# Kernel optimization log

Measured on AMD Instinct MI355X. Metric: run time of the kernel, lower is better.

The kernel has to match this reference:

```python
import jax, jax.numpy as jnp
import numpy as np

VISION_TOKEN_TYPE = 1
HIDDEN = 4096
INTER = 11008


def setup_inputs() -> dict:
    key = jax.random.key(0)
    ks = jax.random.split(key, 8)
    B, L, D, F = 2, 2048, HIDDEN, INTER
    s_in = 1.0 / np.sqrt(D)
    s_mid = 1.0 / np.sqrt(F)
    inp = {
        "hidden_states": jax.random.normal(ks[0], (B, L, D), dtype=jnp.float32),
        "token_type_ids": jax.random.randint(ks[1], (B, L), 0, 2, dtype=jnp.int64),
        # language expert weights (stored as [in, out] for x @ W)
        "lang_gate": jax.random.normal(ks[2], (D, F), dtype=jnp.float32) * s_in,
        "lang_up": jax.random.normal(ks[3], (D, F), dtype=jnp.float32) * s_in,
        "lang_down": jax.random.normal(ks[4], (F, D), dtype=jnp.float32) * s_mid,
        # vision expert weights
        "vis_gate": jax.random.normal(ks[5], (D, F), dtype=jnp.float32) * s_in,
        "vis_up": jax.random.normal(ks[6], (D, F), dtype=jnp.float32) * s_in,
        "vis_down": jax.random.normal(ks[7], (F, D), dtype=jnp.float32) * s_mid,
    }
    return inp


def _swiglu_mlp(x, w_gate, w_up, w_down):
    # x: (B, L, D) -> (B, L, D)
    return (jax.nn.silu(x @ w_gate) * (x @ w_up)) @ w_down


def _vision_mask(token_type_ids):
    # vision token i is one whose type AND next token's type are VISION_TOKEN_TYPE;
    # last position is always language.
    is_vis = token_type_ids == VISION_TOKEN_TYPE
    pair = is_vis[:, :-1] & is_vis[:, 1:]
    return jnp.pad(pair, ((0, 0), (0, 1)), constant_values=False)  # (B, L) bool


def reference(hidden_states, token_type_ids, lang_gate, lang_up, lang_down,
              vis_gate, vis_up, vis_down):
    vision_mask = _vision_mask(token_type_ids)  # (B, L)
    out_vis = _swiglu_mlp(hidden_states, vis_gate, vis_up, vis_down)
    out_lang = _swiglu_mlp(hidden_states, lang_gate, lang_up, lang_down)
    return jnp.where(vision_mask[..., None], out_vis, out_lang)
```

## Files before the change

kernel.cpp:

```cpp
#include <hip/hip_runtime.h>
#include <cstdint>

#define HD 4096
#define FF 11008
#define BB 2
#define LL 2048
#define BL (BB*LL)
#define NN 86
#define MB1 17
#define MB2 17

using bf16x8  = __attribute__((ext_vector_type(8))) __bf16;
using f32x4   = __attribute__((ext_vector_type(4))) float;
using ushort8 = __attribute__((ext_vector_type(8))) unsigned short;

__device__ __forceinline__ int imin(int a, int b) { return a < b ? a : b; }

__device__ __forceinline__ unsigned short f2bf(float f) {
  union { float f; unsigned u; } v; v.f = f;
  unsigned r = v.u + 0x7fffu + ((v.u >> 16) & 1u);
  return (unsigned short)(r >> 16);
}

__device__ __forceinline__ void gld_lds16(const void* g, void* l) {
  __builtin_amdgcn_global_load_lds(
      (__attribute__((address_space(1))) void*)g,
      (__attribute__((address_space(3))) void*)l, 16, 0, 0);
}

__global__ void detect_mode(const int* __restrict__ w, int* __restrict__ flag) {
  int acc = 0;
  for (int i = 1 + 2 * (int)threadIdx.x; i < BL; i += 512) acc |= w[i];
  if (acc != 0) atomicOr(flag, 1);
}

__global__ void mask_compact(const int* __restrict__ w, const int* __restrict__ flag,
                             int* __restrict__ cnts, int* __restrict__ idxL,
                             int* __restrict__ idxV) {
  int i = blockIdx.x * 256 + threadIdx.x;
  if (i >= BL) return;
  int p = i & (LL - 1);
  bool i32 = (*flag != 0);
  int ti = i32 ? w[i] : w[2 * i];
  bool vis = false;
  if (p < LL - 1) {
    int tn = i32 ? w[i + 1] : w[2 * (i + 1)];
    vis = (ti == 1) && (tn == 1);
  }
  if (vis) idxV[atomicAdd(&cnts[1], 1)] = i;
  else     idxL[atomicAdd(&cnts[0], 1)] = i;
}

__global__ void convx(const float* __restrict__ x, unsigned short* __restrict__ xb) {
  size_t i = ((size_t)blockIdx.x * 256 + threadIdx.x) * 8;
  float4 a = *(const float4*)(x + i);
  float4 b = *(const float4*)(x + i + 4);
  ushort8 o;
  o[0] = f2bf(a.x); o[1] = f2bf(a.y); o[2] = f2bf(a.z); o[3] = f2bf(a.w);
  o[4] = f2bf(b.x); o[5] = f2bf(b.y); o[6] = f2bf(b.z); o[7] = f2bf(b.w);
  *(ushort8*)(xb + i) = o;
}

__global__ __launch_bounds__(256) void convTW(const float* __restrict__ in,
                                              unsigned short* __restrict__ out,
                                              int K, int N, int toff) {
  __shared__ unsigned short T[64 * 260];
  const int n0 = blockIdx.x * 256, k0 = blockIdx.y * 64;
  const int t = threadIdx.x, w = t >> 6, l = t & 63;
#pragma unroll
  for (int it = 0; it < 16; ++it) {
    int k = it * 4 + w;
    float4 v = *(const float4*)(in + (size_t)(k0 + k) * N + n0 + l * 4);
    unsigned lo = (unsigned)f2bf(v.x) | ((unsigned)f2bf(v.y) << 16);
    unsigned hi = (unsigned)f2bf(v.z) | ((unsigned)f2bf(v.w) << 16);
    *(uint2*)&T[k * 260 + l * 4] = make_uint2(lo, hi);
  }
  __syncthreads();
  const int gn = n0 + t;
  size_t r = (toff < 0) ? (size_t)gn
                        : (size_t)(((gn >> 4) << 5) + toff + (gn & 15));
  unsigned short* op = out + r * K + k0;
#pragma unroll
  for (int c = 0; c < 8; ++c) {
    ushort8 o;
#pragma unroll
    for (int j = 0; j < 8; ++j) o[j] = T[(c * 8 + j) * 260 + t];
    *(ushort8*)(op + c * 8) = o;
  }
}

#define BAR()  __builtin_amdgcn_s_barrier()
#define VMC(n) asm volatile("s_waitcnt vmcnt(" #n ")" ::: "memory")
#define LGK0() asm volatile("s_waitcnt lgkmcnt(0)" ::: "memory")

#define STG_A(h, kt) { \
  gld_lds16(aptr[h][0] + (size_t)(kt) * 64, &lds[(((kt) & 1) << 14) + ((h) << 13) + w * 512]); \
  gld_lds16(aptr[h][1] + (size_t)(kt) * 64, &lds[(((kt) & 1) << 14) + ((h) << 13) + (w + 8) * 512]); }
#define STG_B(h, kt) { \
  gld_lds16(bptr[h][0] + (size_t)(kt) * 64, &lds[32768 + (((kt) & 1) << 14) + ((h) << 13) + w * 512]); \
  gld_lds16(bptr[h][1] + (size_t)(kt) * 64, &lds[32768 + (((kt) & 1) << 14) + ((h) << 13) + (w + 8) * 512]); }

#define RD_A(s, rh) { _Pragma("unroll") \
  for (int mi = 0; mi < 4; ++mi) { \
    a[mi][0] = *(const bf16x8*)&lds[((s) << 14) + addrA[rh][mi]]; \
    a[mi][1] = *(const bf16x8*)&lds[((s) << 14) + (addrA[rh][mi] ^ 32)]; } }
#define RD_B(s, ch, br) { _Pragma("unroll") \
  for (int ni = 0; ni < 2; ++ni) { \
    br[ni][0] = *(const bf16x8*)&lds[((s) << 14) + addrB[ch][ni]]; \
    br[ni][1] = *(const bf16x8*)&lds[((s) << 14) + (addrB[ch][ni] ^ 32)]; } }

#define MFMA_Q(rh, br, ch) { \
  __builtin_amdgcn_s_setprio(1); \
  _Pragma("unroll") for (int mi = 0; mi < 4; ++mi) \
  _Pragma("unroll") for (int ni = 0; ni < 2; ++ni) { \
    acc[(rh)*4+mi][(ch)*2+ni] = __builtin_amdgcn_mfma_f32_16x16x32_bf16(a[mi][0], br[ni][0], acc[(rh)*4+mi][(ch)*2+ni], 0, 0, 0); \
    acc[(rh)*4+mi][(ch)*2+ni] = __builtin_amdgcn_mfma_f32_16x16x32_bf16(a[mi][1], br[ni][1], acc[(rh)*4+mi][(ch)*2+ni], 0, 0, 0); } \
  __builtin_amdgcn_s_setprio(0); }

#define KLOOP_8PH(KEXT) \
  STG_A(0, 0); STG_A(1, 0); STG_B(0, 0); STG_B(1, 0); \
  STG_B(0, 1); STG_B(1, 1); \
  VMC(4); BAR(); \
  for (int i = 0; i < (KEXT) / 128 - 1; ++i) { \
    const int kt1 = 2 * i + 1, kt2 = 2 * i + 2, kt3 = 2 * i + 3; \
    RD_A(0, 0); RD_B(0, 0, b0); STG_A(0, kt1); BAR(); LGK0(); \
    MFMA_Q(0, b0, 0); BAR(); \
    RD_B(0, 1, b1); STG_A(1, kt1); BAR(); LGK0(); \
    MFMA_Q(0, b1, 1); BAR(); \
    RD_A(0, 1); STG_B(0, kt2); BAR(); LGK0(); \
    MFMA_Q(1, b0, 0); BAR(); \
    STG_B(1, kt2); VMC(4); BAR(); \
    MFMA_Q(1, b1, 1); BAR(); \
    RD_A(1, 0); RD_B(1, 0, b0); STG_A(0, kt2); BAR(); LGK0(); \
    MFMA_Q(0, b0, 0); BAR(); \
    RD_B(1, 1, b1); STG_A(1, kt2); BAR(); LGK0(); \
    MFMA_Q(0, b1, 1); BAR(); \
    RD_A(1, 1); STG_B(0, kt3); BAR(); LGK0(); \
    MFMA_Q(1, b0, 0); BAR(); \
    STG_B(1, kt3); VMC(4); BAR(); \
    MFMA_Q(1, b1, 1); BAR(); \
  } \
  { \
    const int kt1 = (KEXT) / 64 - 1; \
    RD_A(0, 0); RD_B(0, 0, b0); STG_A(0, kt1); BAR(); LGK0(); \
    MFMA_Q(0, b0, 0); BAR(); \
    RD_B(0, 1, b1); STG_A(1, kt1); BAR(); LGK0(); \
    MFMA_Q(0, b1, 1); BAR(); \
    RD_A(0, 1); BAR(); LGK0(); \
    MFMA_Q(1, b0, 0); BAR(); \
    VMC(0); BAR(); \
    MFMA_Q(1, b1, 1); BAR(); \
    RD_A(1, 0); RD_B(1, 0, b0); BAR(); LGK0(); \
    MFMA_Q(0, b0, 0); BAR(); \
    RD_B(1, 1, b1); BAR(); LGK0(); \
    MFMA_Q(0, b1, 1); BAR(); \
    RD_A(1, 1); BAR(); LGK0(); \
    MFMA_Q(1, b0, 0); BAR(); \
    BAR(); \
    MFMA_Q(1, b1, 1); BAR(); \
  }

__global__ __launch_bounds__(512, 2) void gemm1m_8ph(
    const unsigned short* __restrict__ Xb,
    const unsigned short* __restrict__ Wgu0, const unsigned short* __restrict__ Wgu1,
    const int* __restrict__ idxL, const int* __restrict__ idxV,
    const int* __restrict__ cnts, unsigned short* __restrict__ H) {
  const int orig = blockIdx.x;
  const int xcd = orig & 7;
  const int pos = orig >> 3;
  const int wgid = xcd * 183 + pos;
  const int bx = wgid / MB1;
  int mb = wgid - bx * MB1;
  if (bx >= NN) return;
  const int cntL = cnts[0], cntV = cnts[1];
  const int nL = (cntL + 255) >> 8;
  const int* idx; const unsigned short* Wgu; int cnt;
  if (mb < nL) { idx = idxL; Wgu = Wgu0; cnt = cntL; }
  else {
    mb -= nL;
    if (mb >= ((cntV + 255) >> 8)) return;
    idx = idxV; Wgu = Wgu1; cnt = cntV;
  }
  const int m0 = mb << 8;

  __shared__ __align__(16) unsigned short lds[65536];

  const int t = threadIdx.x, l = t & 63, w = t >> 6;
  const int wr = w >> 2, wc = w & 3;
  const int srcswz = (((l & 7) ^ (l >> 3)) << 3);

  const unsigned short* aptr[2][2];
  const unsigned short* bptr[2][2];
#pragma unroll
  for (int h = 0; h < 2; ++h)
#pragma unroll
    for (int j = 0; j < 2; ++j) {
      int r = h * 128 + (w + j * 8) * 8 + (l >> 3);
      int tok = idx[imin(m0 + r, cnt - 1)];
      aptr[h][j] = Xb + (size_t)tok * HD + srcswz;
      bptr[h][j] = Wgu + (size_t)(bx * 256 + r) * HD + srcswz;
    }

  const int koff0 = (((l >> 4) ^ (l & 7)) << 3);
  int addrA[2][4], addrB[2][2];
#pragma unroll
  for (int rh = 0; rh < 2; ++rh)
#pragma unroll
    for (int mi = 0; mi < 4; ++mi)
      addrA[rh][mi] = (wr * 128 + rh * 64 + mi * 16 + (l & 15)) * 64 + koff0;
#pragma unroll
  for (int ch = 0; ch < 2; ++ch)
#pragma unroll
    for (int ni = 0; ni < 2; ++ni)
      addrB[ch][ni] = 32768 + (wc * 64 + ch * 32 + ni * 16 + (l & 15)) * 64 + koff0;

  f32x4 acc[8][4] = {};
  bf16x8 a[4][2], b0[2][2], b1[2][2];

  KLOOP_8PH(HD)

#pragma unroll
  for (int mi = 0; mi < 8; ++mi)
#pragma unroll
    for (int j = 0; j < 4; ++j) {
      int grow = m0 + wr * 128 + mi * 16 + ((l >> 4) << 2) + j;
      if (grow < cnt) {
        int token = idx[grow];
#pragma unroll
        for (int pair = 0; pair < 2; ++pair) {
          float g = acc[mi][pair * 2][j];
          float u = acc[mi][pair * 2 + 1][j];
          float h = (g / (1.f + __expf(-g))) * u;
          int f = bx * 128 + wc * 32 + pair * 16 + (l & 15);
          H[(size_t)token * FF + f] = f2bf(h);
        }
      }
    }
}

__global__ __launch_bounds__(512, 2) void gemm2_8ph(
    const unsigned short* __restrict__ Hh,
    const unsigned short* __restrict__ Wd0, const unsigned short* __restrict__ Wd1,
    const int* __restrict__ idxL, const int* __restrict__ idxV,
    const int* __restrict__ cnts, float* __restrict__ Out) {
  const int orig = blockIdx.x;
  const int xcd = orig & 7;
  const int pos = orig >> 3;
  const int wgid = xcd * ((HD / 256) * MB2 / 8) + pos;
  const int bx = wgid / MB2;
  int mb = wgid - bx * MB2;
  const int cntL = cnts[0], cntV = cnts[1];
  const int nL = (cntL + 255) >> 8;
  const int* idx; const unsigned short* Wd; int cnt;
  if (mb < nL) { idx = idxL; Wd = Wd0; cnt = cntL; }
  else {
    mb -= nL;
    if (mb >= ((cntV + 255) >> 8)) return;
    idx = idxV; Wd = Wd1; cnt = cntV;
  }
  const int m0 = mb << 8;

  __shared__ __align__(16) unsigned short lds[65536];

  const int t = threadIdx.x, l = t & 63, w = t >> 6;
  const int wr = w >> 2, wc = w & 3;
  const int srcswz = (((l & 7) ^ (l >> 3)) << 3);

  const unsigned short* aptr[2][2];
  const unsigned short* bptr[2][2];
#pragma unroll
  for (int h = 0; h < 2; ++h)
#pragma unroll
    for (int j = 0; j < 2; ++j) {
      int r = h * 128 + (w + j * 8) * 8 + (l >> 3);
      int tok = idx[imin(m0 + r, cnt - 1)];
      aptr[h][j] = Hh + (size_t)tok * FF + srcswz;
      bptr[h][j] = Wd + (size_t)(bx * 256 + r) * FF + srcswz;
    }

  const int koff0 = (((l >> 4) ^ (l & 7)) << 3);
  int addrA[2][4], addrB[2][2];
#pragma unroll
  for (int rh = 0; rh < 2; ++rh)
#pragma unroll
    for (int mi = 0; mi < 4; ++mi)
      addrA[rh][mi] = (wr * 128 + rh * 64 + mi * 16 + (l & 15)) * 64 + koff0;
#pragma unroll
  for (int ch = 0; ch < 2; ++ch)
#pragma unroll
    for (int ni = 0; ni < 2; ++ni)
      addrB[ch][ni] = 32768 + (wc * 64 + ch * 32 + ni * 16 + (l & 15)) * 64 + koff0;

  f32x4 acc[8][4] = {};
  bf16x8 a[4][2], b0[2][2], b1[2][2];

  KLOOP_8PH(FF)

#pragma unroll
  for (int mi = 0; mi < 8; ++mi)
#pragma unroll
    for (int j = 0; j < 4; ++j) {
      int grow = m0 + wr * 128 + mi * 16 + ((l >> 4) << 2) + j;
      if (grow < cnt) {
        int token = idx[grow];
        size_t base = (size_t)token * HD + bx * 256 + wc * 64 + (l & 15);
#pragma unroll
        for (int nf = 0; nf < 4; ++nf)
          Out[base + nf * 16] = acc[mi][nf][j];
      }
    }
}

extern "C" void kernel_launch(void* const* d_in, const int* in_sizes, int n_in,
                              void* d_out, int out_size, void* d_ws, size_t ws_size,
                              hipStream_t stream) {
  const float* hs = (const float*)d_in[0];
  const int*   tt = (const int*)d_in[1];
  const float* lg = (const float*)d_in[2];
  const float* lu = (const float*)d_in[3];
  const float* ld = (const float*)d_in[4];
  const float* vg = (const float*)d_in[5];
  const float* vu = (const float*)d_in[6];
  const float* vd = (const float*)d_in[7];
  float* out = (float*)d_out;
  char* ws = (char*)d_ws;

  int* cnts = (int*)ws;
  int* flag = (int*)(ws + 8);
  int* idxL = (int*)(ws + 1024);
  int* idxV = (int*)(ws + 1024 + BL * 4);
  unsigned short* Xb   = (unsigned short*)(ws + 65536);
  unsigned short* Hb   = Xb + (size_t)BL * HD;
  unsigned short* Wgu0 = Hb + (size_t)BL * FF;
  unsigned short* Wgu1 = Wgu0 + (size_t)2 * HD * FF;
  unsigned short* Wd0  = Wgu0;
  unsigned short* Wd1  = Wgu0 + (size_t)HD * FF;

  hipMemsetAsync(ws, 0, 64, stream);
  detect_mode<<<1, 256, 0, stream>>>(tt, flag);
  mask_compact<<<BL / 256, 256, 0, stream>>>(tt, flag, cnts, idxL, idxV);
  convx<<<(BL * HD / 8) / 256, 256, 0, stream>>>(hs, Xb);

  convTW<<<dim3(FF / 256, HD / 64), 256, 0, stream>>>(lg, Wgu0, HD, FF, 0);
  convTW<<<dim3(FF / 256, HD / 64), 256, 0, stream>>>(lu, Wgu0, HD, FF, 16);
  convTW<<<dim3(FF / 256, HD / 64), 256, 0, stream>>>(vg, Wgu1, HD, FF, 0);
  convTW<<<dim3(FF / 256, HD / 64), 256, 0, stream>>>(vu, Wgu1, HD, FF, 16);
  gemm1m_8ph<<<dim3(8 * 183), 512, 0, stream>>>(Xb, Wgu0, Wgu1, idxL, idxV, cnts, Hb);

  convTW<<<dim3(HD / 256, FF / 64), 256, 0, stream>>>(ld, Wd0, FF, HD, -1);
  convTW<<<dim3(HD / 256, FF / 64), 256, 0, stream>>>(vd, Wd1, FF, HD, -1);
  gemm2_8ph<<<dim3((HD / 256) * MB2), 512, 0, stream>>>(Hb, Wd0, Wd1, idxL, idxV, cnts, out);
}
```

Before: 1.580 ms.

## Split-K the down-projection GEMM in two and add a reduction pass

```diff
diff --git a/kernel.cpp b/kernel.cpp
--- a/kernel.cpp
+++ b/kernel.cpp
@@ -9,6 +9,7 @@
 #define NN 86
 #define MB1 17
 #define MB2 17
+#define KS2 5504
 
 using bf16x8  = __attribute__((ext_vector_type(8))) __bf16;
 using f32x4   = __attribute__((ext_vector_type(4))) float;
@@ -61,32 +62,41 @@
   *(ushort8*)(xb + i) = o;
 }
 
-__global__ __launch_bounds__(256) void convTW(const float* __restrict__ in,
-                                              unsigned short* __restrict__ out,
-                                              int K, int N, int toff) {
-  __shared__ unsigned short T[64 * 260];
-  const int n0 = blockIdx.x * 256, k0 = blockIdx.y * 64;
-  const int t = threadIdx.x, w = t >> 6, l = t & 63;
-#pragma unroll
-  for (int it = 0; it < 16; ++it) {
-    int k = it * 4 + w;
-    float4 v = *(const float4*)(in + (size_t)(k0 + k) * N + n0 + l * 4);
-    unsigned lo = (unsigned)f2bf(v.x) | ((unsigned)f2bf(v.y) << 16);
-    unsigned hi = (unsigned)f2bf(v.z) | ((unsigned)f2bf(v.w) << 16);
-    *(uint2*)&T[k * 260 + l * 4] = make_uint2(lo, hi);
+__global__ void convT(const float* __restrict__ in, unsigned short* __restrict__ out,
+                      int K, int N, int toff) {
+  __shared__ unsigned short T[64][65];
+  int n0 = blockIdx.x * 64, k0 = blockIdx.y * 64;
+  int t = threadIdx.x;
+  int cg = (t & 15) * 4;
+  int r0 = t >> 4;
+#pragma unroll
+  for (int it = 0; it < 4; ++it) {
+    int r = r0 + it * 16;
+    float4 v = *(const float4*)(in + (size_t)(k0 + r) * N + n0 + cg);
+    T[cg + 0][r] = f2bf(v.x); T[cg + 1][r] = f2bf(v.y);
+    T[cg + 2][r] = f2bf(v.z); T[cg + 3][r] = f2bf(v.w);
   }
   __syncthreads();
-  const int gn = n0 + t;
-  size_t r = (toff < 0) ? (size_t)gn
-                        : (size_t)(((gn >> 4) << 5) + toff + (gn & 15));
-  unsigned short* op = out + r * K + k0;
-#pragma unroll
-  for (int c = 0; c < 8; ++c) {
+  int nl = t >> 3, kg = t & 7;
+#pragma unroll
+  for (int it = 0; it < 2; ++it) {
+    int n = nl + it * 32;
     ushort8 o;
 #pragma unroll
-    for (int j = 0; j < 8; ++j) o[j] = T[(c * 8 + j) * 260 + t];
-    *(ushort8*)(op + c * 8) = o;
-  }
+    for (int j = 0; j < 8; ++j) o[j] = T[n][kg * 8 + j];
+    int gn = n0 + n;
+    size_t r = (toff < 0) ? (size_t)gn
+                          : (size_t)(((gn >> 4) << 5) + toff + (gn & 15));
+    *(ushort8*)(out + r * K + k0 + kg * 8) = o;
+  }
+}
+
+__global__ void reduce2(const float* __restrict__ P, float* __restrict__ out) {
+  size_t i = ((size_t)blockIdx.x * 256 + threadIdx.x) * 4;
+  float4 a = *(const float4*)(P + i);
+  float4 b = *(const float4*)(P + (size_t)BL * HD + i);
+  float4 o = make_float4(a.x + b.x, a.y + b.y, a.z + b.z, a.w + b.w);
+  *(float4*)(out + i) = o;
 }
 
 #define BAR()  __builtin_amdgcn_s_barrier()
@@ -242,13 +252,15 @@
     const unsigned short* __restrict__ Hh,
     const unsigned short* __restrict__ Wd0, const unsigned short* __restrict__ Wd1,
     const int* __restrict__ idxL, const int* __restrict__ idxV,
-    const int* __restrict__ cnts, float* __restrict__ Out) {
+    const int* __restrict__ cnts, float* __restrict__ P) {
   const int orig = blockIdx.x;
   const int xcd = orig & 7;
   const int pos = orig >> 3;
-  const int wgid = xcd * ((HD / 256) * MB2 / 8) + pos;
-  const int bx = wgid / MB2;
-  int mb = wgid - bx * MB2;
+  const int wgid = xcd * 68 + pos;
+  const int sK = wgid / (16 * MB2);
+  const int rr = wgid - sK * (16 * MB2);
+  const int bx = rr / MB2;
+  int mb = rr - bx * MB2;
   const int cntL = cnts[0], cntV = cnts[1];
   const int nL = (cntL + 255) >> 8;
   const int* idx; const unsigned short* Wd; int cnt;
@@ -259,6 +271,7 @@
     idx = idxV; Wd = Wd1; cnt = cntV;
   }
   const int m0 = mb << 8;
+  const size_t kbase = (size_t)sK * KS2;
 
   __shared__ __align__(16) unsigned short lds[65536];
 
@@ -274,8 +287,8 @@
     for (int j = 0; j < 2; ++j) {
       int r = h * 128 + (w + j * 8) * 8 + (l >> 3);
       int tok = idx[imin(m0 + r, cnt - 1)];
-      aptr[h][j] = Hh + (size_t)tok * FF + srcswz;
-      bptr[h][j] = Wd + (size_t)(bx * 256 + r) * FF + srcswz;
+      aptr[h][j] = Hh + (size_t)tok * FF + kbase + srcswz;
+      bptr[h][j] = Wd + (size_t)(bx * 256 + r) * FF + kbase + srcswz;
     }
 
   const int koff0 = (((l >> 4) ^ (l & 7)) << 3);
@@ -294,8 +307,9 @@
   f32x4 acc[8][4] = {};
   bf16x8 a[4][2], b0[2][2], b1[2][2];
 
-  KLOOP_8PH(FF)
-
+  KLOOP_8PH(KS2)
+
+  float* Pout = P + (size_t)sK * BL * HD;
 #pragma unroll
   for (int mi = 0; mi < 8; ++mi)
 #pragma unroll
@@ -306,7 +320,7 @@
         size_t base = (size_t)token * HD + bx * 256 + wc * 64 + (l & 15);
 #pragma unroll
         for (int nf = 0; nf < 4; ++nf)
-          Out[base + nf * 16] = acc[mi][nf][j];
+          Pout[base + nf * 16] = acc[mi][nf][j];
       }
     }
 }
@@ -335,19 +349,21 @@
   unsigned short* Wgu1 = Wgu0 + (size_t)2 * HD * FF;
   unsigned short* Wd0  = Wgu0;
   unsigned short* Wd1  = Wgu0 + (size_t)HD * FF;
+  float* Pk = (float*)(Wgu0 + (size_t)2 * HD * FF);
 
   hipMemsetAsync(ws, 0, 64, stream);
   detect_mode<<<1, 256, 0, stream>>>(tt, flag);
   mask_compact<<<BL / 256, 256, 0, stream>>>(tt, flag, cnts, idxL, idxV);
   convx<<<(BL * HD / 8) / 256, 256, 0, stream>>>(hs, Xb);
 
-  convTW<<<dim3(FF / 256, HD / 64), 256, 0, stream>>>(lg, Wgu0, HD, FF, 0);
-  convTW<<<dim3(FF / 256, HD / 64), 256, 0, stream>>>(lu, Wgu0, HD, FF, 16);
-  convTW<<<dim3(FF / 256, HD / 64), 256, 0, stream>>>(vg, Wgu1, HD, FF, 0);
-  convTW<<<dim3(FF / 256, HD / 64), 256, 0, stream>>>(vu, Wgu1, HD, FF, 16);
+  convT<<<dim3(FF / 64, HD / 64), 256, 0, stream>>>(lg, Wgu0, HD, FF, 0);
+  convT<<<dim3(FF / 64, HD / 64), 256, 0, stream>>>(lu, Wgu0, HD, FF, 16);
+  convT<<<dim3(FF / 64, HD / 64), 256, 0, stream>>>(vg, Wgu1, HD, FF, 0);
+  convT<<<dim3(FF / 64, HD / 64), 256, 0, stream>>>(vu, Wgu1, HD, FF, 16);
   gemm1m_8ph<<<dim3(8 * 183), 512, 0, stream>>>(Xb, Wgu0, Wgu1, idxL, idxV, cnts, Hb);
 
-  convTW<<<dim3(HD / 256, FF / 64), 256, 0, stream>>>(ld, Wd0, FF, HD, -1);
-  convTW<<<dim3(HD / 256, FF / 64), 256, 0, stream>>>(vd, Wd1, FF, HD, -1);
-  gemm2_8ph<<<dim3((HD / 256) * MB2), 512, 0, stream>>>(Hb, Wd0, Wd1, idxL, idxV, cnts, out);
-}
+  convT<<<dim3(HD / 64, FF / 64), 256, 0, stream>>>(ld, Wd0, FF, HD, -1);
+  convT<<<dim3(HD / 64, FF / 64), 256, 0, stream>>>(vd, Wd1, FF, HD, -1);
+  gemm2_8ph<<<dim3(8 * 68), 512, 0, stream>>>(Hb, Wd0, Wd1, idxL, idxV, cnts, Pk);
+  reduce2<<<dim3((size_t)BL * HD / 4 / 256), 256, 0, stream>>>(Pk, out);
+}
```

Result: faster. 1.447 ms (-8.4%).
